# Optimization experiments

Hardware: AMD Instinct MI355X
Metric: run time of the kernel (lower is better)

## Reference

```python
import jax, jax.numpy as jnp
import numpy as np

D_K = 64

def setup_inputs() -> dict:
    key = jax.random.key(0)
    kq, kk, kv = jax.random.split(key, 3)
    shape = (2, 16, 2048, D_K)  # [B, H, S, d_k]
    q = jax.random.normal(kq, shape, dtype=jnp.float32)
    k = jax.random.normal(kk, shape, dtype=jnp.float32)
    v = jax.random.normal(kv, shape, dtype=jnp.float32)
    return {"q": q, "k": k, "v": v}

def reference(q, k, v):
    # score = q @ k^T / sqrt(d_k)  -> [B, H, S, S]
    scale = 1.0 / np.sqrt(D_K).astype(np.float32)
    score = jnp.einsum("bhqd,bhkd->bhqk", q, k) * scale
    attn = jax.nn.softmax(score, axis=-1)
    # dropout is identity in eval mode
    out = jnp.einsum("bhqk,bhkd->bhqd", attn, v)
    return out
```

## Files before the change

kernel.cpp:

```cpp
#include <hip/hip_runtime.h>
#include <hip/hip_bf16.h>
#include <math.h>
#include <stdint.h>


#define S_LEN 2048
#define DK 64
#define QW 32
#define QBLK 64
#define KVBLK 64
#define NT (S_LEN / KVBLK)
#define KVSPLIT 2
#define NTG (NT / KVSPLIT)
#define LOG2E 1.44269504088896340736f
#define MSTAT 8.0f

typedef __attribute__((ext_vector_type(16))) float f32x16;
typedef __attribute__((ext_vector_type(8)))  __bf16 bf16x8;
typedef __attribute__((ext_vector_type(4)))  __bf16 bf16x4;
typedef __attribute__((ext_vector_type(4)))  uint32_t u32x4;

union frag_cast { u32x4 u; bf16x8 h; };

__device__ __forceinline__ uint32_t cvt_pk_bf16(float lo, float hi) {
    uint32_t r;
    asm("v_cvt_pk_bf16_f32 %0, %1, %2" : "=v"(r) : "v"(lo), "v"(hi));
    return r;
}
__device__ __forceinline__ void perm32swap(uint32_t& a, uint32_t& b) {
    asm volatile("v_permlane32_swap_b32 %0, %1" : "+v"(a), "+v"(b));
}
__device__ __forceinline__ void load_lds16(const __bf16* g, __bf16* l) {
    __builtin_amdgcn_global_load_lds(
        (const __attribute__((address_space(1))) void*)g,
        (__attribute__((address_space(3))) void*)l, 16, 0, 0);
}
__device__ __forceinline__ bf16x8 pack8(float4 a, float4 b) {
    bf16x8 f;
    f[0] = (__bf16)a.x; f[1] = (__bf16)a.y; f[2] = (__bf16)a.z; f[3] = (__bf16)a.w;
    f[4] = (__bf16)b.x; f[5] = (__bf16)b.y; f[6] = (__bf16)b.z; f[7] = (__bf16)b.w;
    return f;
}

__global__ __launch_bounds__(256)
void prep_pack(const float* __restrict__ Kg, const float* __restrict__ Vg,
               __bf16* __restrict__ Kimg, __bf16* __restrict__ Vimg)
{
    __shared__ float Vs[64 * 65];
    const int tid = threadIdx.x;
    const int t = blockIdx.x, bh = blockIdx.y;
    const size_t ibase = ((size_t)bh * S_LEN + (size_t)t * 64) * DK;
    const size_t obase = ((size_t)bh * NT + t) * 4096;

    #pragma unroll
    for (int u0 = 0; u0 < 2; ++u0) {
        const int u = tid + 256 * u0;
        const int f = u >> 6, lane = u & 63;
        const int sp = f >> 1, kt2 = f & 1;
        const int row = kt2 * 32 + (lane & 31);
        const int col = 16 * sp + 8 * (lane >> 5);
        const float* src = Kg + ibase + row * 64 + col;
        float4 a = *(const float4*)(src);
        float4 b = *(const float4*)(src + 4);
        *(bf16x8*)(Kimg + obase + (size_t)u * 8) = pack8(a, b);
    }

    {
        const int r = tid >> 2, c0 = (tid & 3) * 16;
        const float* src = Vg + ibase + r * 64 + c0;
        #pragma unroll
        for (int m = 0; m < 4; ++m) {
            float4 x = *(const float4*)(src + 4 * m);
            float* dst = &Vs[r * 65 + c0 + 4 * m];
            dst[0] = x.x; dst[1] = x.y; dst[2] = x.z; dst[3] = x.w;
        }
    }
    __syncthreads();
    #pragma unroll
    for (int u0 = 0; u0 < 2; ++u0) {
        const int u = tid + 256 * u0;
        const int g = u >> 6, lane = u & 63;
        const int ks = g >> 1, dt = g & 1;
        const int k0 = 16 * ks + 8 * (lane >> 5);
        const int d  = dt * 32 + (lane & 31);
        bf16x8 wv;
        #pragma unroll
        for (int i = 0; i < 8; ++i) wv[i] = (__bf16)Vs[(k0 + i) * 65 + d];
        *(bf16x8*)(Vimg + obase + (size_t)u * 8) = wv;
    }
}

__global__ __launch_bounds__(256, 4)
void attn_fwd_lds(const float* __restrict__ Qg, const __bf16* __restrict__ Kimg,
                  const __bf16* __restrict__ Vimg, float* __restrict__ Og)
{
    __shared__ __align__(16) unsigned char smem[33280];
    __bf16* KlBase = (__bf16*)smem;
    float* O1p = (float*)smem;
    float* l1a = (float*)(smem + 16384);

    const int tid  = threadIdx.x;
    const int lane = tid & 63;
    const int wv   = tid >> 6;
    const int qg   = wv & 1;
    const int g    = wv >> 1;
    const int l31  = lane & 31;
    const int hi   = lane >> 5;

    int qt, bh;
    {
        const int lin = blockIdx.y * gridDim.x + blockIdx.x;
        if (gridDim.x * gridDim.y == 1024) {
            const int xcd = lin & 7, slot = lin >> 3;
            bh = xcd * 4 + (slot >> 5);
            qt = slot & 31;
        } else { qt = blockIdx.x; bh = blockIdx.y; }
    }

    const size_t base = (size_t)bh * (S_LEN * DK);
    const int q0g = qt * QBLK + qg * QW;

    bf16x8 qf[4];
    {
        const float sc = 0.125f * LOG2E;
        const float* qrow = Qg + base + (size_t)(q0g + l31) * DK;
        #pragma unroll
        for (int sp = 0; sp < 4; ++sp) {
            const int d0 = 16 * sp + 8 * hi;
            float4 a = *(const float4*)(qrow + d0);
            float4 b = *(const float4*)(qrow + d0 + 4);
            bf16x8 f;
            f[0] = (__bf16)(a.x * sc); f[1] = (__bf16)(a.y * sc);
            f[2] = (__bf16)(a.z * sc); f[3] = (__bf16)(a.w * sc);
            f[4] = (__bf16)(b.x * sc); f[5] = (__bf16)(b.y * sc);
            f[6] = (__bf16)(b.z * sc); f[7] = (__bf16)(b.w * sc);
            qf[sp] = f;
        }
    }

    f32x16 acc0 = {}, acc1 = {};
    float l_run = 0.f;

    const __bf16* kbase = Kimg + (size_t)bh * NT * 4096;
    const __bf16* vw = Vimg + ((size_t)bh * NT + (size_t)g * NTG) * 4096 + lane * 8;
    const int loff = lane * 8;
    const int t0 = g * NTG;

    auto stageK = [&](int tl, int b) {
        const __bf16* kt = kbase + (size_t)(t0 + tl) * 4096 + lane * 8;
        __bf16* kd = KlBase + (size_t)(g * 2 + b) * 4096;
        #pragma unroll
        for (int c = 0; c < 4; ++c) {
            const int chunk = c * 2 + qg;
            load_lds16(kt + chunk * 512, kd + chunk * 512);
        }
    };

    auto doks = [&](float e0, float e1, float e2, float e3,
                    float e4, float e5, float e6, float e7,
                    bf16x8 w0, bf16x8 w1) {
        const float p0 = __builtin_amdgcn_exp2f(e0);
        const float p1 = __builtin_amdgcn_exp2f(e1);
        const float p2 = __builtin_amdgcn_exp2f(e2);
        const float p3 = __builtin_amdgcn_exp2f(e3);
        const float p4 = __builtin_amdgcn_exp2f(e4);
        const float p5 = __builtin_amdgcn_exp2f(e5);
        const float p6 = __builtin_amdgcn_exp2f(e6);
        const float p7 = __builtin_amdgcn_exp2f(e7);
        l_run += ((p0 + p1) + (p2 + p3)) + ((p4 + p5) + (p6 + p7));
        uint32_t wa = cvt_pk_bf16(p0, p1);
        uint32_t wb = cvt_pk_bf16(p2, p3);
        uint32_t wc = cvt_pk_bf16(p4, p5);
        uint32_t wd = cvt_pk_bf16(p6, p7);
        perm32swap(wa, wc);
        perm32swap(wb, wd);
        frag_cast pa;
        pa.u = (u32x4){wa, wb, wc, wd};
        __builtin_amdgcn_s_setprio(1);
        acc0 = __builtin_amdgcn_mfma_f32_32x32x16_bf16(pa.h, w0, acc0, 0, 0, 0);
        acc1 = __builtin_amdgcn_mfma_f32_32x32x16_bf16(pa.h, w1, acc1, 0, 0, 0);
        __builtin_amdgcn_s_setprio(0);
    };

    stageK(0, 0);
    __syncthreads();

    int cur = 0;
    #pragma unroll 1
    for (int tl = 0; tl < NTG; ++tl) {
        if (tl + 1 < NTG) stageK(tl + 1, cur ^ 1);

        const __bf16* Kc = KlBase + (size_t)(g * 2 + cur) * 4096;
        const __bf16* vt = vw + (size_t)tl * 4096;

        f32x16 s0, s1;
        #pragma unroll
        for (int j = 0; j < 16; ++j) { s0[j] = -MSTAT; s1[j] = -MSTAT; }
        __builtin_amdgcn_s_setprio(1);
        #pragma unroll
        for (int sp = 0; sp < 4; ++sp) {
            bf16x8 kb0 = *(const bf16x8*)(&Kc[(sp * 2 + 0) * 512 + loff]);
            bf16x8 kb1 = *(const bf16x8*)(&Kc[(sp * 2 + 1) * 512 + loff]);
            s0 = __builtin_amdgcn_mfma_f32_32x32x16_bf16(kb0, qf[sp], s0, 0, 0, 0);
            s1 = __builtin_amdgcn_mfma_f32_32x32x16_bf16(kb1, qf[sp], s1, 0, 0, 0);
        }
        __builtin_amdgcn_s_setprio(0);

        bf16x8 va0 = *(const bf16x8*)(vt);
        bf16x8 va1 = *(const bf16x8*)(vt + 512);
        bf16x8 va2 = *(const bf16x8*)(vt + 1024);
        bf16x8 va3 = *(const bf16x8*)(vt + 1536);

        doks(s0[0], s0[1], s0[2], s0[3], s0[4], s0[5], s0[6], s0[7], va0, va1);
        doks(s0[8], s0[9], s0[10], s0[11], s0[12], s0[13], s0[14], s0[15], va2, va3);

        bf16x8 vb0 = *(const bf16x8*)(vt + 2048);
        bf16x8 vb1 = *(const bf16x8*)(vt + 2560);
        bf16x8 vb2 = *(const bf16x8*)(vt + 3072);
        bf16x8 vb3 = *(const bf16x8*)(vt + 3584);

        doks(s1[0], s1[1], s1[2], s1[3], s1[4], s1[5], s1[6], s1[7], vb0, vb1);
        doks(s1[8], s1[9], s1[10], s1[11], s1[12], s1[13], s1[14], s1[15], vb2, vb3);

        __syncthreads();
        cur ^= 1;
    }

    l_run += __shfl_xor(l_run, 32);

    if (g == 1) {
        #pragma unroll
        for (int r = 0; r < 16; ++r) {
            const int ql = (r & 3) + 8 * (r >> 2) + 4 * hi;
            const int row = qg * 32 + ql;
            O1p[row * 64 + l31]      = acc0[r];
            O1p[row * 64 + 32 + l31] = acc1[r];
        }
        if (hi == 0) l1a[qg * 32 + l31] = l_run;
    }
    __syncthreads();

    if (g == 0) {
        float* op = Og + base;
        #pragma unroll
        for (int r = 0; r < 16; ++r) {
            const int ql = (r & 3) + 8 * (r >> 2) + 4 * hi;
            const int row = qg * 32 + ql;
            const float lr = __shfl(l_run, ql) + l1a[row];
            const float invl = 1.0f / lr;
            const float o0 = acc0[r] + O1p[row * 64 + l31];
            const float o1 = acc1[r] + O1p[row * 64 + 32 + l31];
            const size_t orow = (size_t)(q0g + ql) * DK;
            op[orow + l31]      = o0 * invl;
            op[orow + 32 + l31] = o1 * invl;
        }
    }
}

__global__ __launch_bounds__(256, 2)
void attn_fwd_fb(const float* __restrict__ Qg, const float* __restrict__ Kg,
                 const float* __restrict__ Vg, float* __restrict__ Og)
{
    __shared__ __align__(16) __bf16 Kl[2][64 * 64];
    __shared__ __align__(16) __bf16 Vt[2][64 * 64];

    const int tid = threadIdx.x;
    const int lane = tid & 63;
    const int w   = tid >> 6;
    const int l31 = lane & 31;
    const int hi  = lane >> 5;

    const int qt = blockIdx.x;
    const int bh = blockIdx.y;
    const size_t base = (size_t)bh * (S_LEN * DK);
    const int q0g = qt * 128 + w * QW;

    bf16x8 qf[4];
    {
        const float sc = 0.125f * LOG2E;
        const float* qrow = Qg + base + (size_t)(q0g + l31) * DK;
        #pragma unroll
        for (int sp = 0; sp < 4; ++sp) {
            const int d0 = 16 * sp + 8 * hi;
            float4 a = *(const float4*)(qrow + d0);
            float4 b = *(const float4*)(qrow + d0 + 4);
            bf16x8 f;
            f[0] = (__bf16)(a.x * sc); f[1] = (__bf16)(a.y * sc);
            f[2] = (__bf16)(a.z * sc); f[3] = (__bf16)(a.w * sc);
            f[4] = (__bf16)(b.x * sc); f[5] = (__bf16)(b.y * sc);
            f[6] = (__bf16)(b.z * sc); f[7] = (__bf16)(b.w * sc);
            qf[sp] = f;
        }
    }

    f32x16 acc0 = {}, acc1 = {};
    float m_run = -INFINITY, l_run = 0.f;

    float4 kpre[4];
    float  vpre[4][4];
    const int vd  = tid & 63;
    const int vkq = tid >> 6;

    auto issueLoads = [&](int t) {
        const int kv0 = t * KVBLK;
        #pragma unroll
        for (int i = 0; i < 4; ++i) {
            const int idx = tid + 256 * i;
            const int r = idx >> 4, c = idx & 15;
            kpre[i] = *(const float4*)(Kg + base + (size_t)(kv0 + r) * DK + c * 4);
        }
        #pragma unroll
        for (int i = 0; i < 4; ++i) {
            const int k0 = vkq * 4 + 16 * i;
            const float* vp = Vg + base + (size_t)(kv0 + k0) * DK + vd;
            vpre[i][0] = vp[0];      vpre[i][1] = vp[DK];
            vpre[i][2] = vp[2 * DK]; vpre[i][3] = vp[3 * DK];
        }
    };
    auto writeTile = [&](int b) {
        #pragma unroll
        for (int i = 0; i < 4; ++i) {
            const int idx = tid + 256 * i;
            const int r = idx >> 4, c = idx & 15;
            bf16x4 pk;
            pk[0] = (__bf16)kpre[i].x; pk[1] = (__bf16)kpre[i].y;
            pk[2] = (__bf16)kpre[i].z; pk[3] = (__bf16)kpre[i].w;
            *(bf16x4*)(&Kl[b][r * 64 + ((c * 4) ^ ((r & 7) << 3))]) = pk;
        }
        #pragma unroll
        for (int i = 0; i < 4; ++i) {
            const int k0 = vkq * 4 + 16 * i;
            bf16x4 pv;
            pv[0] = (__bf16)vpre[i][0]; pv[1] = (__bf16)vpre[i][1];
            pv[2] = (__bf16)vpre[i][2]; pv[3] = (__bf16)vpre[i][3];
            *(bf16x4*)(&Vt[b][vd * 64 + (k0 ^ ((vd & 7) << 3))]) = pv;
        }
    };

    issueLoads(0);
    writeTile(0);
    __syncthreads();

    int cur = 0;
    #pragma unroll 1
    for (int t = 0; t < NT; ++t) {
        if (t + 1 < NT) issueLoads(t + 1);

        f32x16 s0 = {}, s1 = {};
        #pragma unroll
        for (int sp = 0; sp < 4; ++sp) {
            #pragma unroll
            for (int kt2 = 0; kt2 < 2; ++kt2) {
                const int krow = kt2 * 32 + l31;
                const int eo = krow * 64 + ((16 * sp + 8 * hi) ^ ((krow & 7) << 3));
                bf16x8 kb = *(const bf16x8*)(&Kl[cur][eo]);
                if (kt2 == 0) s0 = __builtin_amdgcn_mfma_f32_32x32x16_bf16(kb, qf[sp], s0, 0, 0, 0);
                else          s1 = __builtin_amdgcn_mfma_f32_32x32x16_bf16(kb, qf[sp], s1, 0, 0, 0);
            }
        }

        float vmax = -INFINITY;
        #pragma unroll
        for (int j = 0; j < 16; ++j) vmax = fmaxf(vmax, s0[j]);
        #pragma unroll
        for (int j = 0; j < 16; ++j) vmax = fmaxf(vmax, s1[j]);
        vmax = fmaxf(vmax, __shfl_xor(vmax, 32));

        if (!__all(vmax - m_run <= 8.0f)) {
            const float mnew = fmaxf(m_run, vmax);
            const float alpha = __builtin_amdgcn_exp2f(m_run - mnew);
            m_run = mnew;
            l_run *= alpha;
            #pragma unroll
            for (int r = 0; r < 16; ++r) {
                const int ql = (r & 3) + 8 * (r >> 2) + 4 * hi;
                const float ar = __shfl(alpha, ql + (hi << 5));
                acc0[r] *= ar;
                acc1[r] *= ar;
            }
        }

        float rs = 0.f;
        #pragma unroll
        for (int j = 0; j < 16; ++j) { const float p = __builtin_amdgcn_exp2f(s0[j] - m_run); s0[j] = p; rs += p; }
        #pragma unroll
        for (int j = 0; j < 16; ++j) { const float p = __builtin_amdgcn_exp2f(s1[j] - m_run); s1[j] = p; rs += p; }
        rs += __shfl_xor(rs, 32);
        l_run += rs;

        frag_cast pa[4];
        #pragma unroll
        for (int b2 = 0; b2 < 2; ++b2) {
            #pragma unroll
            for (int st = 0; st < 2; ++st) {
                uint32_t wa, wb, wc, wd;
                if (b2 == 0) {
                    wa = cvt_pk_bf16(s0[8 * st + 0], s0[8 * st + 1]);
                    wb = cvt_pk_bf16(s0[8 * st + 2], s0[8 * st + 3]);
                    wc = cvt_pk_bf16(s0[8 * st + 4], s0[8 * st + 5]);
                    wd = cvt_pk_bf16(s0[8 * st + 6], s0[8 * st + 7]);
                } else {
                    wa = cvt_pk_bf16(s1[8 * st + 0], s1[8 * st + 1]);
                    wb = cvt_pk_bf16(s1[8 * st + 2], s1[8 * st + 3]);
                    wc = cvt_pk_bf16(s1[8 * st + 4], s1[8 * st + 5]);
                    wd = cvt_pk_bf16(s1[8 * st + 6], s1[8 * st + 7]);
                }
                perm32swap(wa, wc);
                perm32swap(wb, wd);
                pa[2 * b2 + st].u = (u32x4){wa, wb, wc, wd};
            }
        }

        #pragma unroll
        for (int ks = 0; ks < 4; ++ks) {
            #pragma unroll
            for (int dt = 0; dt < 2; ++dt) {
                const int d = dt * 32 + l31;
                const int eo = d * 64 + ((16 * ks + 8 * hi) ^ ((d & 7) << 3));
                bf16x8 vb = *(const bf16x8*)(&Vt[cur][eo]);
                if (dt == 0) acc0 = __builtin_amdgcn_mfma_f32_32x32x16_bf16(pa[ks].h, vb, acc0, 0, 0, 0);
                else         acc1 = __builtin_amdgcn_mfma_f32_32x32x16_bf16(pa[ks].h, vb, acc1, 0, 0, 0);
            }
        }

        if (t + 1 < NT) writeTile(cur ^ 1);
        __syncthreads();
        cur ^= 1;
    }

    float* op = Og + base;
    #pragma unroll
    for (int r = 0; r < 16; ++r) {
        const int ql = (r & 3) + 8 * (r >> 2) + 4 * hi;
        const float lr = __shfl(l_run, ql + (hi << 5));
        const float invl = 1.0f / lr;
        const size_t row = (size_t)(q0g + ql) * DK;
        op[row + l31]      = acc0[r] * invl;
        op[row + 32 + l31] = acc1[r] * invl;
    }
}

extern "C" void kernel_launch(void* const* d_in, const int* in_sizes, int n_in,
                              void* d_out, int out_size, void* d_ws, size_t ws_size,
                              hipStream_t stream) {
    const float* q = (const float*)d_in[0];
    const float* k = (const float*)d_in[1];
    const float* v = (const float*)d_in[2];
    float* o = (float*)d_out;
    const int bh = in_sizes[0] / (S_LEN * DK);

    const size_t img_bytes = (size_t)bh * NT * 4096 * sizeof(__bf16);
    if (ws_size >= 2 * img_bytes) {
        __bf16* Kimg = (__bf16*)d_ws;
        __bf16* Vimg = (__bf16*)((char*)d_ws + img_bytes);
        prep_pack<<<dim3(NT, bh), dim3(256), 0, stream>>>(k, v, Kimg, Vimg);
        attn_fwd_lds<<<dim3(S_LEN / QBLK, bh), dim3(256), 0, stream>>>(q, Kimg, Vimg, o);
    } else {
        attn_fwd_fb<<<dim3(S_LEN / 128, bh), dim3(256), 0, stream>>>(q, k, v, o);
    }
}
```

Baseline: 61.99 us.

## Replace LDS-staged K tiles with register double-buffered global loads

The attention kernel no longer stages K tiles through LDS with async copies and per-tile barriers. Each wave now loads its K fragments straight from the packed global image into two register buffers, prefetching the next tile while the current one is processed. This removes the LDS round trip and the per-iteration __syncthreads. In exchange the two waves sharing a KV group load K redundantly from global/L2, register pressure rises, and launch bounds drop from 4 to 3 blocks per SIMD-unit group.

```diff
diff --git a/kernel.cpp b/kernel.cpp
--- a/kernel.cpp
+++ b/kernel.cpp
@@ -90,14 +90,12 @@
     }
 }
 
-__global__ __launch_bounds__(256, 4)
-void attn_fwd_lds(const float* __restrict__ Qg, const __bf16* __restrict__ Kimg,
-                  const __bf16* __restrict__ Vimg, float* __restrict__ Og)
+__global__ __launch_bounds__(256, 3)
+void attn_fwd_reg2(const float* __restrict__ Qg, const __bf16* __restrict__ Kimg,
+                   const __bf16* __restrict__ Vimg, float* __restrict__ Og)
 {
-    __shared__ __align__(16) unsigned char smem[33280];
-    __bf16* KlBase = (__bf16*)smem;
-    float* O1p = (float*)smem;
-    float* l1a = (float*)(smem + 16384);
+    __shared__ __align__(16) float O1p[64 * 64];
+    __shared__ float l1a[64];
 
     const int tid  = threadIdx.x;
     const int lane = tid & 63;
@@ -141,20 +139,8 @@
     f32x16 acc0 = {}, acc1 = {};
     float l_run = 0.f;
 
-    const __bf16* kbase = Kimg + (size_t)bh * NT * 4096;
+    const __bf16* kw = Kimg + ((size_t)bh * NT + (size_t)g * NTG) * 4096 + lane * 8;
     const __bf16* vw = Vimg + ((size_t)bh * NT + (size_t)g * NTG) * 4096 + lane * 8;
-    const int loff = lane * 8;
-    const int t0 = g * NTG;
-
-    auto stageK = [&](int tl, int b) {
-        const __bf16* kt = kbase + (size_t)(t0 + tl) * 4096 + lane * 8;
-        __bf16* kd = KlBase + (size_t)(g * 2 + b) * 4096;
-        #pragma unroll
-        for (int c = 0; c < 4; ++c) {
-            const int chunk = c * 2 + qg;
-            load_lds16(kt + chunk * 512, kd + chunk * 512);
-        }
-    };
 
     auto doks = [&](float e0, float e1, float e2, float e3,
                     float e4, float e5, float e6, float e7,
@@ -182,48 +168,42 @@
         __builtin_amdgcn_s_setprio(0);
     };
 
-    stageK(0, 0);
-    __syncthreads();
-
-    int cur = 0;
-    #pragma unroll 1
-    for (int tl = 0; tl < NTG; ++tl) {
-        if (tl + 1 < NTG) stageK(tl + 1, cur ^ 1);
-
-        const __bf16* Kc = KlBase + (size_t)(g * 2 + cur) * 4096;
-        const __bf16* vt = vw + (size_t)tl * 4096;
-
+    auto doTile = [&](int tl, bf16x8* kvC, bf16x8* kvN, bool pre) {
         f32x16 s0, s1;
         #pragma unroll
         for (int j = 0; j < 16; ++j) { s0[j] = -MSTAT; s1[j] = -MSTAT; }
         __builtin_amdgcn_s_setprio(1);
         #pragma unroll
         for (int sp = 0; sp < 4; ++sp) {
-            bf16x8 kb0 = *(const bf16x8*)(&Kc[(sp * 2 + 0) * 512 + loff]);
-            bf16x8 kb1 = *(const bf16x8*)(&Kc[(sp * 2 + 1) * 512 + loff]);
-            s0 = __builtin_amdgcn_mfma_f32_32x32x16_bf16(kb0, qf[sp], s0, 0, 0, 0);
-            s1 = __builtin_amdgcn_mfma_f32_32x32x16_bf16(kb1, qf[sp], s1, 0, 0, 0);
+            s0 = __builtin_amdgcn_mfma_f32_32x32x16_bf16(kvC[2 * sp + 0], qf[sp], s0, 0, 0, 0);
+            s1 = __builtin_amdgcn_mfma_f32_32x32x16_bf16(kvC[2 * sp + 1], qf[sp], s1, 0, 0, 0);
         }
         __builtin_amdgcn_s_setprio(0);
 
-        bf16x8 va0 = *(const bf16x8*)(vt);
-        bf16x8 va1 = *(const bf16x8*)(vt + 512);
-        bf16x8 va2 = *(const bf16x8*)(vt + 1024);
-        bf16x8 va3 = *(const bf16x8*)(vt + 1536);
-
-        doks(s0[0], s0[1], s0[2], s0[3], s0[4], s0[5], s0[6], s0[7], va0, va1);
-        doks(s0[8], s0[9], s0[10], s0[11], s0[12], s0[13], s0[14], s0[15], va2, va3);
-
-        bf16x8 vb0 = *(const bf16x8*)(vt + 2048);
-        bf16x8 vb1 = *(const bf16x8*)(vt + 2560);
-        bf16x8 vb2 = *(const bf16x8*)(vt + 3072);
-        bf16x8 vb3 = *(const bf16x8*)(vt + 3584);
-
-        doks(s1[0], s1[1], s1[2], s1[3], s1[4], s1[5], s1[6], s1[7], vb0, vb1);
-        doks(s1[8], s1[9], s1[10], s1[11], s1[12], s1[13], s1[14], s1[15], vb2, vb3);
-
-        __syncthreads();
-        cur ^= 1;
+        const __bf16* vt = vw + (size_t)tl * 4096;
+        bf16x8 vv[8];
+        #pragma unroll
+        for (int f = 0; f < 8; ++f) vv[f] = *(const bf16x8*)(vt + f * 512);
+        if (pre) {
+            const __bf16* kn = kw + (size_t)(tl + 1) * 4096;
+            #pragma unroll
+            for (int f = 0; f < 8; ++f) kvN[f] = *(const bf16x8*)(kn + f * 512);
+        }
+
+        doks(s0[0], s0[1], s0[2], s0[3], s0[4], s0[5], s0[6], s0[7], vv[0], vv[1]);
+        doks(s0[8], s0[9], s0[10], s0[11], s0[12], s0[13], s0[14], s0[15], vv[2], vv[3]);
+        doks(s1[0], s1[1], s1[2], s1[3], s1[4], s1[5], s1[6], s1[7], vv[4], vv[5]);
+        doks(s1[8], s1[9], s1[10], s1[11], s1[12], s1[13], s1[14], s1[15], vv[6], vv[7]);
+    };
+
+    bf16x8 kvA[8], kvB[8];
+    #pragma unroll
+    for (int f = 0; f < 8; ++f) kvA[f] = *(const bf16x8*)(kw + f * 512);
+
+    #pragma unroll 1
+    for (int t2 = 0; t2 < NTG; t2 += 2) {
+        doTile(t2,     kvA, kvB, true);
+        doTile(t2 + 1, kvB, kvA, t2 + 2 < NTG);
     }
 
     l_run += __shfl_xor(l_run, 32);
@@ -454,7 +434,7 @@
         __bf16* Kimg = (__bf16*)d_ws;
         __bf16* Vimg = (__bf16*)((char*)d_ws + img_bytes);
         prep_pack<<<dim3(NT, bh), dim3(256), 0, stream>>>(k, v, Kimg, Vimg);
-        attn_fwd_lds<<<dim3(S_LEN / QBLK, bh), dim3(256), 0, stream>>>(q, Kimg, Vimg, o);
+        attn_fwd_reg2<<<dim3(S_LEN / QBLK, bh), dim3(256), 0, stream>>>(q, Kimg, Vimg, o);
     } else {
         attn_fwd_fb<<<dim3(S_LEN / 128, bh), dim3(256), 0, stream>>>(q, k, v, o);
     }
```

After: 226.1 us. 3.65x slower.
